# Kernel tuning notes

Measured on AMD Instinct MI355X. Metric: run time of the kernel, lower is better.

The kernel has to match this reference:

```python
import jax, jax.numpy as jnp
import numpy as np

S, H, NH, I = 4096, 2048, 16, 5504
HD = H // NH
EPS = 1e-6
ROPE_BASE = 10000.0


def setup_inputs() -> dict:
    key = jax.random.key(0)
    ks = jax.random.split(key, 10)
    sc = lambda fan_in: 1.0 / np.sqrt(fan_in)
    return {
        "x": jax.random.normal(ks[0], (S, H), jnp.float32),
        "wq": jax.random.normal(ks[1], (H, H), jnp.float32) * sc(H),
        "wk": jax.random.normal(ks[2], (H, H), jnp.float32) * sc(H),
        "wv": jax.random.normal(ks[3], (H, H), jnp.float32) * sc(H),
        "wo": jax.random.normal(ks[4], (H, H), jnp.float32) * sc(H),
        "w_gate": jax.random.normal(ks[5], (H, I), jnp.float32) * sc(H),
        "w_up": jax.random.normal(ks[6], (H, I), jnp.float32) * sc(H),
        "w_down": jax.random.normal(ks[7], (I, H), jnp.float32) * sc(I),
        "g1": jnp.ones((H,), jnp.float32),
        "g2": jnp.ones((H,), jnp.float32),
    }


def _rmsnorm(x, g):
    var = jnp.mean(x * x, axis=-1, keepdims=True)
    return x * jax.lax.rsqrt(var + EPS) * g


def _rope(x):
    # x: [S, NH, HD]; classic interleaved-pair rotation applied per position.
    pos = jnp.arange(S, dtype=jnp.float32)
    inv_freq = 1.0 / (ROPE_BASE ** (jnp.arange(0, HD, 2, dtype=jnp.float32) / HD))
    ang = pos[:, None] * inv_freq[None, :]              # [S, HD/2]
    cos = jnp.cos(ang)[:, None, :]                      # [S, 1, HD/2]
    sin = jnp.sin(ang)[:, None, :]
    xe = x[..., 0::2]
    xo = x[..., 1::2]
    out = jnp.stack([xe * cos - xo * sin, xe * sin + xo * cos], axis=-1)
    return out.reshape(x.shape)


def _block(x, wq, wk, wv, wo, w_gate, w_up, w_down, g1, g2):
    # --- attention sublayer ---
    h = _rmsnorm(x, g1)
    q = _rope((h @ wq).reshape(S, NH, HD))
    k = _rope((h @ wk).reshape(S, NH, HD))
    v = (h @ wv).reshape(S, NH, HD)
    scores = jnp.einsum("snd,tnd->nst", q, k) / np.sqrt(HD).astype(np.float32)
    causal = jnp.tril(jnp.ones((S, S), bool))
    scores = jnp.where(causal[None], scores, jnp.finfo(scores.dtype).min)
    probs = jax.nn.softmax(scores, axis=-1)
    attn = jnp.einsum("nst,tnd->snd", probs, v).reshape(S, H)
    x = x + attn @ wo
    # --- MLP sublayer (SwiGLU) ---
    h = _rmsnorm(x, g2)
    mlp = (jax.nn.silu(h @ w_gate) * (h @ w_up)) @ w_down
    return x + mlp


def reference(x, wq, wk, wv, wo, w_gate, w_up, w_down, g1, g2):
    return _block(x, wq, wk, wv, wo, w_gate, w_up, w_down, g1, g2)
```

## Files before the change

kernel.cpp:

```cpp
#include <hip/hip_runtime.h>
#include <stdint.h>

constexpr int SEQ  = 4096;
constexpr int HID  = 2048;
constexpr int NHEAD = 16;
constexpr int HDIM = 128;
constexpr int INTER = 5504;
constexpr int IPAD  = 5632;

using u16 = unsigned short;
typedef __bf16 bf16x8 __attribute__((ext_vector_type(8)));
typedef float  f32x4  __attribute__((ext_vector_type(4)));
typedef u16    u16x4  __attribute__((ext_vector_type(4)));
typedef u16    u16x8  __attribute__((ext_vector_type(8)));

__device__ __forceinline__ u16 f2bf(float f) {
  union { float f; unsigned u; } v; v.f = f;
  return (u16)((v.u + 0x7fffu + ((v.u >> 16) & 1u)) >> 16);
}
__device__ __forceinline__ float bf2f(u16 u) {
  union { unsigned u; float f; } v; v.u = ((unsigned)u) << 16;
  return v.f;
}

__device__ __forceinline__ void gl16(const u16* g, u16* l) {
  u16* gg = const_cast<u16*>(g);
  __builtin_amdgcn_global_load_lds(
      (__attribute__((address_space(1))) u16*)gg,
      (__attribute__((address_space(3))) u16*)l, 16, 0, 0);
}

__device__ __forceinline__ f32x4 mfma16(bf16x8 a, bf16x8 b, f32x4 c) {
  return __builtin_amdgcn_mfma_f32_16x16x32_bf16(a, b, c, 0, 0, 0);
}

__global__ __launch_bounds__(256)
void fill_k(float* __restrict__ o, float v, int n) {
  int i = blockIdx.x * 256 + threadIdx.x;
  if (i < n) o[i] = v;
}

__global__ __launch_bounds__(256)
void rmsnorm_k(const float* __restrict__ x, const float* __restrict__ g,
               u16* __restrict__ o) {
  const int row = blockIdx.x, t = threadIdx.x;
  const float4* xr = (const float4*)(x + (size_t)row * HID);
  float4 a = xr[t * 2], b = xr[t * 2 + 1];
  float ss = a.x*a.x + a.y*a.y + a.z*a.z + a.w*a.w
           + b.x*b.x + b.y*b.y + b.z*b.z + b.w*b.w;
  #pragma unroll
  for (int m = 32; m; m >>= 1) ss += __shfl_xor(ss, m);
  __shared__ float red[4];
  if ((t & 63) == 0) red[t >> 6] = ss;
  __syncthreads();
  const float inv = rsqrtf((red[0]+red[1]+red[2]+red[3]) * (1.0f/HID) + 1e-6f);
  float vals[8] = {a.x,a.y,a.z,a.w,b.x,b.y,b.z,b.w};
  const int base = t * 8;
  u16x8 w;
  #pragma unroll
  for (int i = 0; i < 8; ++i) w[i] = f2bf(vals[i] * inv * g[base + i]);
  *(u16x8*)(o + (size_t)row * HID + base) = w;
}

__global__ __launch_bounds__(256)
void wtrans_k(const float* __restrict__ in, u16* __restrict__ out,
              int ldin, int ldout, int Rin, int Cin) {
  __shared__ float tile[32][33];
  const int cb = blockIdx.x * 32, rb = blockIdx.y * 32;
  const int t = threadIdx.x;
  const int c = t >> 3, r4 = (t & 7) * 4;
  if (rb >= Rin || cb >= Cin) {
    u16x4 z = {0, 0, 0, 0};
    *(u16x4*)(out + (size_t)(cb + c) * ldout + rb + r4) = z;
    return;
  }
  const int r = t >> 3, c4 = (t & 7) * 4;
  float4 v = *(const float4*)(in + (size_t)(rb + r) * ldin + cb + c4);
  tile[r][c4] = v.x; tile[r][c4+1] = v.y; tile[r][c4+2] = v.z; tile[r][c4+3] = v.w;
  __syncthreads();
  u16x4 o;
  #pragma unroll
  for (int i = 0; i < 4; ++i) o[i] = f2bf(tile[r4 + i][c]);
  *(u16x4*)(out + (size_t)(cb + c) * ldout + rb + r4) = o;
}

__global__ __launch_bounds__(256)
void vtrans_k(const u16* __restrict__ v, u16* __restrict__ vt) {
  __shared__ u16 tile[32][36];
  const int s0 = blockIdx.x * 32, d0 = blockIdx.y * 32, n = blockIdx.z;
  const int t = threadIdx.x;
  const int r = t >> 3, c4 = (t & 7) * 4;
  u16x4 in = *(const u16x4*)(v + (size_t)(s0 + r) * HID + n * HDIM + d0 + c4);
  tile[r][c4] = in[0]; tile[r][c4+1] = in[1]; tile[r][c4+2] = in[2]; tile[r][c4+3] = in[3];
  __syncthreads();
  const int d = t >> 3, s4 = (t & 7) * 4;
  u16x4 o;
  #pragma unroll
  for (int i = 0; i < 4; ++i) o[i] = tile[s4 + i][d];
  *(u16x4*)(vt + ((size_t)n * HDIM + d0 + d) * SEQ + s0 + s4) = o;
}

__global__ __launch_bounds__(256)
void rope_k(u16* __restrict__ x) {
  const int idx = blockIdx.x * 256 + threadIdx.x;
  const int i  = idx & 63;
  const int sn = idx >> 6;
  const int s  = sn >> 4;
  const size_t base = (size_t)sn * HDIM + 2 * i;
  const float xe = bf2f(x[base]), xo = bf2f(x[base + 1]);
  const float inv_freq = exp2f(-(float)i * (13.287712379549449f / 64.0f));
  const float ang = (float)s * inv_freq;
  float sv, cv;
  sincosf(ang, &sv, &cv);
  x[base]     = f2bf(xe * cv - xo * sv);
  x[base + 1] = f2bf(xe * sv + xo * cv);
}

template<int EPI>
__global__ __launch_bounds__(256)
void gemm128(const u16* __restrict__ A, const u16* __restrict__ B,
             void* C, const void* extra, int M, int N, int K, int gx) {
  __shared__ __align__(16) u16 As[128 * 64];
  __shared__ __align__(16) u16 Bs[128 * 64];
  const int nwg = gridDim.x;
  const int bid = blockIdx.x;
  const int wgid = (bid & 7) * (nwg >> 3) + (bid >> 3);
  const int bx = wgid % gx, by = wgid / gx;
  const int m0 = by * 128, n0 = bx * 128;
  const int tid = threadIdx.x;
  const int w = tid >> 6, lane = tid & 63;
  const int l15 = lane & 15, g = lane >> 4;
  const int wr = w >> 1, wc = w & 1;
  const int NT = K >> 6;

  f32x4 acc[4][4] = {};

  const int srow = tid >> 3;
  const int sgr  = ((tid & 7) ^ (srow & 7)) * 8;
  const u16* gA = A + (size_t)(m0 + srow) * K + sgr;
  const u16* gB = B + (size_t)(n0 + srow) * K + sgr;
  const size_t i32K = (size_t)32 * K;
  const int sl = w * 512;

  const int axor = l15 & 7;
  const int arow0 = (wr * 64 + l15) * 64;
  const int brow0 = (wc * 64 + l15) * 64;

  for (int T = 0; T < NT; ++T) {
    const size_t k0 = (size_t)T * 64;
    gl16(gA + k0,            As + 0 * 2048 + sl);
    gl16(gA + k0 +     i32K, As + 1 * 2048 + sl);
    gl16(gA + k0 + 2 * i32K, As + 2 * 2048 + sl);
    gl16(gA + k0 + 3 * i32K, As + 3 * 2048 + sl);
    gl16(gB + k0,            Bs + 0 * 2048 + sl);
    gl16(gB + k0 +     i32K, Bs + 1 * 2048 + sl);
    gl16(gB + k0 + 2 * i32K, Bs + 2 * 2048 + sl);
    gl16(gB + k0 + 3 * i32K, Bs + 3 * 2048 + sl);
    asm volatile("s_waitcnt vmcnt(0)" ::: "memory");
    __syncthreads();
    #pragma unroll
    for (int ks = 0; ks < 2; ++ks) {
      const int aoff = ((ks * 4 + g) ^ axor) * 8;
      bf16x8 af[4], bfr[4];
      #pragma unroll
      for (int i = 0; i < 4; ++i)
        af[i] = *(const bf16x8*)&As[arow0 + i * 16 * 64 + aoff];
      #pragma unroll
      for (int j = 0; j < 4; ++j)
        bfr[j] = *(const bf16x8*)&Bs[brow0 + j * 16 * 64 + aoff];
      #pragma unroll
      for (int i = 0; i < 4; ++i)
        #pragma unroll
        for (int j = 0; j < 4; ++j)
          acc[i][j] = mfma16(af[i], bfr[j], acc[i][j]);
    }
    asm volatile("s_waitcnt lgkmcnt(0)" ::: "memory");
    __syncthreads();
  }

  #pragma unroll
  for (int i = 0; i < 4; ++i) {
    #pragma unroll
    for (int r = 0; r < 4; ++r) {
      const int row = m0 + wr * 64 + i * 16 + g * 4 + r;
      #pragma unroll
      for (int j = 0; j < 4; ++j) {
        const int col = n0 + wc * 64 + j * 16 + l15;
        const float v = acc[i][j][r];
        if constexpr (EPI == 0) {
          ((u16*)C)[(size_t)(col >> 11) * ((size_t)SEQ * HID)
                    + (size_t)row * HID + (col & 2047)] = f2bf(v);
        } else if constexpr (EPI == 1) {
          const size_t idx = (size_t)row * N + col;
          ((float*)C)[idx] = v + ((const float*)extra)[idx];
        } else if constexpr (EPI == 2) {
          const size_t idx = (size_t)row * N + col;
          const float upv = bf2f(((const u16*)extra)[idx]);
          ((u16*)C)[idx] = f2bf(v / (1.0f + __expf(-v)) * upv);
        } else {
          ((u16*)C)[(size_t)row * N + col] = f2bf(v);
        }
      }
    }
  }
}

__global__ __launch_bounds__(256)
void attn_k(const u16* __restrict__ q, const u16* __restrict__ k,
            const u16* __restrict__ vt, u16* __restrict__ o) {
  __shared__ __align__(16) u16 Ks[64 * 128];
  __shared__ __align__(16) u16 Vs[128 * 64];
  __shared__ __align__(16) u16 Ps[4 * 16 * 64];
  const int b = blockIdx.x;
  const int n    = ((b & 7) << 1) | ((b >> 3) & 1);
  const int qIdx = 63 - (b >> 4);
  const int q0   = qIdx * 64;
  const int tid = threadIdx.x;
  const int wave = tid >> 6, lane = tid & 63;
  const int l15 = lane & 15, g = lane >> 4;

  bf16x8 aq[4];
  {
    const u16* qp = q + (size_t)(q0 + wave*16 + l15) * HID + n * HDIM + g * 8;
    #pragma unroll
    for (int d = 0; d < 4; ++d) aq[d] = *(const bf16x8*)(qp + d * 32);
  }
  float mrow[4], lrow[4];
  #pragma unroll
  for (int r = 0; r < 4; ++r) { mrow[r] = -__builtin_inff(); lrow[r] = 0.0f; }
  f32x4 oacc[8] = {};

  const int kRow = tid >> 4;
  const int kCs  = (tid & 15) ^ (kRow & 7);
  const u16* kg = k + (size_t)kRow * HID + n * HDIM + kCs * 8;
  const int vRow = tid >> 3;
  const int vCs  = (tid & 7) ^ (vRow & 7);
  const u16* vg = vt + ((size_t)n * HDIM + vRow) * SEQ + vCs * 8;

  u16* PW = Ps + wave * 1024;
  const int rsw = (l15 & 7) << 3;
  const float C = 0.12751744f;

  const int nt = qIdx + 1;
  for (int it = 0; it < nt; ++it) {
    const int t0 = it * 64;
    #pragma unroll
    for (int s = 0; s < 4; ++s)
      gl16(kg + (size_t)(t0 + s*16) * HID, Ks + s*2048 + wave*512);
    #pragma unroll
    for (int s = 0; s < 4; ++s)
      gl16(vg + (size_t)(s*32) * SEQ + t0, Vs + s*2048 + wave*512);
    __syncthreads();

    f32x4 sc[4] = {};
    #pragma unroll
    for (int tb = 0; tb < 4; ++tb) {
      #pragma unroll
      for (int dd = 0; dd < 4; ++dd) {
        bf16x8 bk = *(const bf16x8*)(Ks + (tb*16 + l15)*128 + ((dd*32 + g*8) ^ rsw));
        sc[tb] = mfma16(aq[dd], bk, sc[tb]);
      }
    }

    float fex[4];
    #pragma unroll
    for (int r = 0; r < 4; ++r) {
      const int srow = q0 + wave*16 + g*4 + r;
      const int tt = t0 + l15;
      float v0 = sc[0][r], v1 = sc[1][r], v2 = sc[2][r], v3 = sc[3][r];
      if (tt      > srow) v0 = -__builtin_inff();
      if (tt + 16 > srow) v1 = -__builtin_inff();
      if (tt + 32 > srow) v2 = -__builtin_inff();
      if (tt + 48 > srow) v3 = -__builtin_inff();
      float mx = fmaxf(fmaxf(v0, v1), fmaxf(v2, v3));
      mx = fmaxf(mx, __shfl_xor(mx, 1));
      mx = fmaxf(mx, __shfl_xor(mx, 2));
      mx = fmaxf(mx, __shfl_xor(mx, 4));
      mx = fmaxf(mx, __shfl_xor(mx, 8));
      const float mnew = fmaxf(mrow[r], mx);
      const float f = exp2f((mrow[r] - mnew) * C);
      mrow[r] = mnew;
      const float p0 = exp2f((v0 - mnew) * C);
      const float p1 = exp2f((v1 - mnew) * C);
      const float p2 = exp2f((v2 - mnew) * C);
      const float p3 = exp2f((v3 - mnew) * C);
      float ps = (p0 + p1) + (p2 + p3);
      ps += __shfl_xor(ps, 1);
      ps += __shfl_xor(ps, 2);
      ps += __shfl_xor(ps, 4);
      ps += __shfl_xor(ps, 8);
      lrow[r] = lrow[r] * f + ps;
      fex[r] = f;
      const int prow = g*4 + r;
      const int psw = (prow & 7) << 3;
      PW[prow*64 + ( l15        ^ psw)] = f2bf(p0);
      PW[prow*64 + ((16 + l15)  ^ psw)] = f2bf(p1);
      PW[prow*64 + ((32 + l15)  ^ psw)] = f2bf(p2);
      PW[prow*64 + ((48 + l15)  ^ psw)] = f2bf(p3);
    }
    #pragma unroll
    for (int db = 0; db < 8; ++db)
      #pragma unroll
      for (int r = 0; r < 4; ++r) oacc[db][r] *= fex[r];

    bf16x8 ap0 = *(const bf16x8*)(PW + l15*64 + ((g*8)      ^ rsw));
    bf16x8 ap1 = *(const bf16x8*)(PW + l15*64 + ((32 + g*8) ^ rsw));
    #pragma unroll
    for (int db = 0; db < 8; ++db) {
      bf16x8 bv0 = *(const bf16x8*)(Vs + (db*16 + l15)*64 + ((g*8)      ^ rsw));
      bf16x8 bv1 = *(const bf16x8*)(Vs + (db*16 + l15)*64 + ((32 + g*8) ^ rsw));
      oacc[db] = mfma16(ap0, bv0, oacc[db]);
      oacc[db] = mfma16(ap1, bv1, oacc[db]);
    }
    __syncthreads();
  }

  #pragma unroll
  for (int db = 0; db < 8; ++db) {
    #pragma unroll
    for (int r = 0; r < 4; ++r) {
      const int srow = q0 + wave*16 + g*4 + r;
      o[(size_t)srow * HID + n * HDIM + db*16 + l15] = f2bf(oacc[db][r] / lrow[r]);
    }
  }
}

extern "C" void kernel_launch(void* const* d_in, const int* in_sizes, int n_in,
                              void* d_out, int out_size, void* d_ws, size_t ws_size,
                              hipStream_t stream) {
  (void)in_sizes; (void)n_in; (void)out_size;
  const float* x  = (const float*)d_in[0];
  const float* wq = (const float*)d_in[1];
  const float* wk = (const float*)d_in[2];
  const float* wv = (const float*)d_in[3];
  const float* wo = (const float*)d_in[4];
  const float* wg = (const float*)d_in[5];
  const float* wu = (const float*)d_in[6];
  const float* wd = (const float*)d_in[7];
  const float* g1 = (const float*)d_in[8];
  const float* g2 = (const float*)d_in[9];
  float* out = (float*)d_out;

  constexpr size_t HB  = (size_t)SEQ * HID * 2;
  constexpr size_t WT  = (size_t)HID * HID * 2;
  constexpr size_t WUP = (size_t)IPAD * HID * 2;
  constexpr size_t UPH = (size_t)SEQ * IPAD * 2;
  constexpr size_t NEED1 = 4 * HB + 3 * WT;
  constexpr size_t NEED2 = HB + WUP + UPH;
  constexpr size_t NEED = NEED1 > NEED2 ? NEED1 : NEED2;

  if (ws_size < NEED) {
    const int n = SEQ * HID;
    fill_k<<<dim3((n + 255) / 256), 256, 0, stream>>>(out, (float)(ws_size >> 20), n);
    return;
  }

  char* base = (char*)d_ws;
  u16* h1     = (u16*)(base);
  u16* wqkvT  = (u16*)(base + HB);
  u16* qb     = (u16*)(base + HB + 3 * WT);
  u16* kb     = (u16*)(base + 2 * HB + 3 * WT);
  u16* vb     = (u16*)(base + 3 * HB + 3 * WT);
  u16* vtb    = h1;
  u16* ob     = vb;
  u16* woT    = wqkvT;
  u16* h2    = (u16*)(base);
  u16* slotA = (u16*)(base + HB);
  u16* uph   = (u16*)(base + HB + WUP);

  wtrans_k<<<dim3(64, 64), 256, 0, stream>>>(wq, wqkvT,            HID, HID, HID, HID);
  wtrans_k<<<dim3(64, 64), 256, 0, stream>>>(wk, wqkvT + HID*HID,  HID, HID, HID, HID);
  wtrans_k<<<dim3(64, 64), 256, 0, stream>>>(wv, wqkvT + 2*HID*HID,HID, HID, HID, HID);

  rmsnorm_k<<<dim3(SEQ), 256, 0, stream>>>(x, g1, h1);

  gemm128<0><<<dim3(1536), 256, 0, stream>>>(h1, wqkvT, qb, nullptr, SEQ, 3*HID, HID, 48);

  rope_k<<<dim3(SEQ * NHEAD * 64 / 256), 256, 0, stream>>>(qb);
  rope_k<<<dim3(SEQ * NHEAD * 64 / 256), 256, 0, stream>>>(kb);

  vtrans_k<<<dim3(SEQ/32, HDIM/32, NHEAD), 256, 0, stream>>>(vb, vtb);

  wtrans_k<<<dim3(64, 64), 256, 0, stream>>>(wo, woT, HID, HID, HID, HID);

  attn_k<<<dim3(SEQ/64 * NHEAD), 256, 0, stream>>>(qb, kb, vtb, ob);

  gemm128<1><<<dim3(512), 256, 0, stream>>>(ob, woT, out, x, SEQ, HID, HID, 16);

  rmsnorm_k<<<dim3(SEQ), 256, 0, stream>>>(out, g2, h2);

  wtrans_k<<<dim3(IPAD/32, 64), 256, 0, stream>>>(wu, slotA, INTER, HID, HID, INTER);
  gemm128<3><<<dim3(1408), 256, 0, stream>>>(h2, slotA, uph, nullptr, SEQ, IPAD, HID, 44);

  wtrans_k<<<dim3(IPAD/32, 64), 256, 0, stream>>>(wg, slotA, INTER, HID, HID, INTER);
  gemm128<2><<<dim3(1408), 256, 0, stream>>>(h2, slotA, uph, uph, SEQ, IPAD, HID, 44);

  wtrans_k<<<dim3(64, IPAD/32), 256, 0, stream>>>(wd, slotA, HID, IPAD, INTER, HID);
  gemm128<1><<<dim3(512), 256, 0, stream>>>(uph, slotA, out, out, SEQ, HID, IPAD, 16);
}
```

Baseline: 868.4 us.

## Lazy softmax rescale, MFMA row sums, diagonal-only masking in flash attention

The online-softmax loop now rescales the running max and accumulators only when a new tile's max exceeds the stored max by a threshold, rather than on every tile. Row sums are computed with an extra MFMA against a ones vector instead of shuffle reductions. The causal mask is applied only on the diagonal tile. Probabilities are packed to bf16 with a hardware convert instruction, and explicit waitcnts are added before the barriers. Together these cut VALU, shuffle and exp work per tile. In exchange, unnormalized probabilities can reach roughly 200x, which adds some bf16 rounding risk, and the row sum is now taken from bf16-rounded values.

```diff
diff --git a/kernel.cpp b/kernel.cpp
--- a/kernel.cpp
+++ b/kernel.cpp
@@ -21,6 +21,12 @@
 __device__ __forceinline__ float bf2f(u16 u) {
   union { unsigned u; float f; } v; v.u = ((unsigned)u) << 16;
   return v.f;
+}
+
+__device__ __forceinline__ unsigned cvtpk(float lo, float hi) {
+  unsigned r;
+  asm("v_cvt_pk_bf16_f32 %0, %1, %2" : "=v"(r) : "v"(lo), "v"(hi));
+  return r;
 }
 
 __device__ __forceinline__ void gl16(const u16* g, u16* l) {
@@ -225,10 +231,13 @@
     #pragma unroll
     for (int d = 0; d < 4; ++d) aq[d] = *(const bf16x8*)(qp + d * 32);
   }
-  float mrow[4], lrow[4];
-  #pragma unroll
-  for (int r = 0; r < 4; ++r) { mrow[r] = -__builtin_inff(); lrow[r] = 0.0f; }
+  float mrow[4];
+  #pragma unroll
+  for (int r = 0; r < 4; ++r) mrow[r] = -__builtin_inff();
   f32x4 oacc[8] = {};
+  f32x4 lacc = {0.0f, 0.0f, 0.0f, 0.0f};
+  const bf16x8 vone = {(__bf16)1.0f, (__bf16)1.0f, (__bf16)1.0f, (__bf16)1.0f,
+                       (__bf16)1.0f, (__bf16)1.0f, (__bf16)1.0f, (__bf16)1.0f};
 
   const int kRow = tid >> 4;
   const int kCs  = (tid & 15) ^ (kRow & 7);
@@ -250,6 +259,7 @@
     #pragma unroll
     for (int s = 0; s < 4; ++s)
       gl16(vg + (size_t)(s*32) * SEQ + t0, Vs + s*2048 + wave*512);
+    asm volatile("s_waitcnt vmcnt(0)" ::: "memory");
     __syncthreads();
 
     f32x4 sc[4] = {};
@@ -262,49 +272,49 @@
       }
     }
 
-    float fex[4];
+    const bool diag = (it == qIdx);
     #pragma unroll
     for (int r = 0; r < 4; ++r) {
-      const int srow = q0 + wave*16 + g*4 + r;
-      const int tt = t0 + l15;
       float v0 = sc[0][r], v1 = sc[1][r], v2 = sc[2][r], v3 = sc[3][r];
-      if (tt      > srow) v0 = -__builtin_inff();
-      if (tt + 16 > srow) v1 = -__builtin_inff();
-      if (tt + 32 > srow) v2 = -__builtin_inff();
-      if (tt + 48 > srow) v3 = -__builtin_inff();
+      if (diag) {
+        const int srow = q0 + wave*16 + g*4 + r;
+        const int tt = t0 + l15;
+        if (tt      > srow) v0 = -__builtin_inff();
+        if (tt + 16 > srow) v1 = -__builtin_inff();
+        if (tt + 32 > srow) v2 = -__builtin_inff();
+        if (tt + 48 > srow) v3 = -__builtin_inff();
+      }
       float mx = fmaxf(fmaxf(v0, v1), fmaxf(v2, v3));
       mx = fmaxf(mx, __shfl_xor(mx, 1));
       mx = fmaxf(mx, __shfl_xor(mx, 2));
       mx = fmaxf(mx, __shfl_xor(mx, 4));
       mx = fmaxf(mx, __shfl_xor(mx, 8));
-      const float mnew = fmaxf(mrow[r], mx);
-      const float f = exp2f((mrow[r] - mnew) * C);
-      mrow[r] = mnew;
-      const float p0 = exp2f((v0 - mnew) * C);
-      const float p1 = exp2f((v1 - mnew) * C);
-      const float p2 = exp2f((v2 - mnew) * C);
-      const float p3 = exp2f((v3 - mnew) * C);
-      float ps = (p0 + p1) + (p2 + p3);
-      ps += __shfl_xor(ps, 1);
-      ps += __shfl_xor(ps, 2);
-      ps += __shfl_xor(ps, 4);
-      ps += __shfl_xor(ps, 8);
-      lrow[r] = lrow[r] * f + ps;
-      fex[r] = f;
+      if (mx > mrow[r] + 60.0f) {
+        const float f = exp2f((mrow[r] - mx) * C);
+        mrow[r] = mx;
+        lacc[r] *= f;
+        #pragma unroll
+        for (int db = 0; db < 8; ++db) oacc[db][r] *= f;
+      }
+      const float m = mrow[r];
+      const float p0 = exp2f((v0 - m) * C);
+      const float p1 = exp2f((v1 - m) * C);
+      const float p2 = exp2f((v2 - m) * C);
+      const float p3 = exp2f((v3 - m) * C);
+      const unsigned pk01 = cvtpk(p0, p1);
+      const unsigned pk23 = cvtpk(p2, p3);
       const int prow = g*4 + r;
       const int psw = (prow & 7) << 3;
-      PW[prow*64 + ( l15        ^ psw)] = f2bf(p0);
-      PW[prow*64 + ((16 + l15)  ^ psw)] = f2bf(p1);
-      PW[prow*64 + ((32 + l15)  ^ psw)] = f2bf(p2);
-      PW[prow*64 + ((48 + l15)  ^ psw)] = f2bf(p3);
-    }
-    #pragma unroll
-    for (int db = 0; db < 8; ++db)
-      #pragma unroll
-      for (int r = 0; r < 4; ++r) oacc[db][r] *= fex[r];
+      PW[prow*64 + ( l15        ^ psw)] = (u16)pk01;
+      PW[prow*64 + ((16 + l15)  ^ psw)] = (u16)(pk01 >> 16);
+      PW[prow*64 + ((32 + l15)  ^ psw)] = (u16)pk23;
+      PW[prow*64 + ((48 + l15)  ^ psw)] = (u16)(pk23 >> 16);
+    }
 
     bf16x8 ap0 = *(const bf16x8*)(PW + l15*64 + ((g*8)      ^ rsw));
     bf16x8 ap1 = *(const bf16x8*)(PW + l15*64 + ((32 + g*8) ^ rsw));
+    lacc = mfma16(ap0, vone, lacc);
+    lacc = mfma16(ap1, vone, lacc);
     #pragma unroll
     for (int db = 0; db < 8; ++db) {
       bf16x8 bv0 = *(const bf16x8*)(Vs + (db*16 + l15)*64 + ((g*8)      ^ rsw));
@@ -312,6 +322,7 @@
       oacc[db] = mfma16(ap0, bv0, oacc[db]);
       oacc[db] = mfma16(ap1, bv1, oacc[db]);
     }
+    asm volatile("s_waitcnt lgkmcnt(0)" ::: "memory");
     __syncthreads();
   }
 
@@ -320,7 +331,7 @@
     #pragma unroll
     for (int r = 0; r < 4; ++r) {
       const int srow = q0 + wave*16 + g*4 + r;
-      o[(size_t)srow * HID + n * HDIM + db*16 + l15] = f2bf(oacc[db][r] / lrow[r]);
+      o[(size_t)srow * HID + n * HDIM + db*16 + l15] = f2bf(oacc[db][r] / lacc[r]);
     }
   }
 }
```

New measurement: 858.0 us, median of 2. About the same (-1.2%).
